# Kernel tuning notes

Hardware: AMD Instinct MI355X
Metric: run time of the kernel (lower is better)

Reference implementation:

```python
import jax, jax.numpy as jnp
import numpy as np
import math

D_MODEL = 1024
NUM_HEADS = 16
D_K = D_MODEL // NUM_HEADS
MAX_LEN = 2048
B, S = 2, 1024


def setup_inputs() -> dict:
    key = jax.random.key(0)
    ks = jax.random.split(key, 10)
    lin_scale = 1.0 / math.sqrt(D_MODEL)
    # torch Linear: weight (out, in), y = x @ W.T + b
    Wq = jax.random.uniform(ks[0], (D_MODEL, D_MODEL), jnp.float32, -lin_scale, lin_scale)
    Wk = jax.random.uniform(ks[1], (D_MODEL, D_MODEL), jnp.float32, -lin_scale, lin_scale)
    Wv = jax.random.uniform(ks[2], (D_MODEL, D_MODEL), jnp.float32, -lin_scale, lin_scale)
    Wo = jax.random.uniform(ks[3], (D_MODEL, D_MODEL), jnp.float32, -lin_scale, lin_scale)
    bq = jnp.zeros((D_MODEL,), jnp.float32)
    bk = jnp.zeros((D_MODEL,), jnp.float32)
    bv = jnp.zeros((D_MODEL,), jnp.float32)
    bo = jnp.zeros((D_MODEL,), jnp.float32)
    # xavier_uniform for Er (max_len, d_k)
    er_bound = math.sqrt(6.0 / (MAX_LEN + D_K))
    Er = jax.random.uniform(ks[4], (MAX_LEN, D_K), jnp.float32, -er_bound, er_bound)
    x = jax.random.normal(ks[5], (B, S, D_MODEL), jnp.float32)
    return {"x": x, "Wq": Wq, "bq": bq, "Wk": Wk, "bk": bk,
            "Wv": Wv, "bv": bv, "Wo": Wo, "bo": bo, "Er": Er}


def reference(x, Wq, bq, Wk, bk, Wv, bv, Wo, bo, Er):
    Bsz, Slen, Dm = x.shape
    H, dk = NUM_HEADS, D_K

    def proj(W, b):
        y = jnp.einsum('bsd,ed->bse', x, W) + b
        return y.reshape(Bsz, Slen, H, dk).transpose(0, 2, 1, 3)  # (B,H,S,dk)

    Q = proj(Wq, bq)
    K = proj(Wk, bk)
    V = proj(Wv, bv)

    # content-content scores
    AC = jnp.einsum('bhid,bhjd->bhij', Q, K)  # (B,H,S,S)

    # relative position embeddings for distances S-1 .. -(S-1)
    rel_pos = jnp.arange(Slen - 1, -Slen, -1)  # (2S-1,)
    idx = rel_pos + (Slen - 1)                 # map to 0..2S-2 (requires 2S-1 <= max_len)
    Er_emb = Er[idx]                           # (2S-1, dk)
    BD_full = jnp.einsum('bhid,md->bhim', Q, Er_emb)  # (B,H,S,2S-1)

    # relative shift: final[i,j] = BD_full[i, S-1 - i + j] (column for distance i-j)
    i_idx = jnp.arange(Slen)[:, None]                  # (S,1)
    m_idx = (Slen - 1) - i_idx + jnp.arange(Slen)[None, :]  # (S,S)
    BD = BD_full[:, :, i_idx, m_idx]                   # (B,H,S,S)

    scores = (AC + BD) / math.sqrt(dk)
    attn = jax.nn.softmax(scores, axis=-1)  # dropout is identity at eval
    out = jnp.einsum('bhij,bhjd->bhid', attn, V)       # (B,H,S,dk)
    out = out.transpose(0, 2, 1, 3).reshape(Bsz, Slen, Dm)
    return jnp.einsum('bsd,ed->bse', out, Wo) + bo
```

## Files before the change

kernel.cpp:

```cpp
#include <hip/hip_runtime.h>
#include <hip/hip_bf16.h>
#include <math.h>

#define D_MODEL 1024
#define NUM_HEADS 16
#define D_K 64
#define SEQ 1024
#define BATCH 2

typedef __hip_bfloat16 bf16;
typedef __bf16 bf16x8 __attribute__((ext_vector_type(8)));
typedef __bf16 bf16x4 __attribute__((ext_vector_type(4)));
typedef float floatx4 __attribute__((ext_vector_type(4)));

__device__ __forceinline__ floatx4 mfma16(bf16x8 a, bf16x8 b, floatx4 c) {
    return __builtin_amdgcn_mfma_f32_16x16x32_bf16(a, b, c, 0, 0, 0);
}

__global__ void detect_dtype_kernel(const void* __restrict__ x, int* __restrict__ flag) {
    __shared__ int cnt[256];
    const float* xf = (const float*)x;
    const int tid = threadIdx.x;
    int sane = 0;
    for (int i = tid; i < 4096; i += 256) {
        float v = xf[i];
        float a = fabsf(v);
        if (v == 0.0f || (a > 1e-8f && a < 1e8f)) sane++;
    }
    cnt[tid] = sane;
    __syncthreads();
    for (int s = 128; s > 0; s >>= 1) {
        if (tid < s) cnt[tid] += cnt[tid + s];
        __syncthreads();
    }
    if (tid == 0) flag[0] = (cnt[0] > 3686) ? 1 : 0;
}

struct ConvSrcs { const void* p[10]; };

__global__ __launch_bounds__(256) void convert_all_kernel(ConvSrcs srcs,
                                                          bf16* __restrict__ dstbase,
                                                          const int* __restrict__ flag) {
    const long long e = ((long long)blockIdx.x * 256 + threadIdx.x) * 8;
    int seg; long long base;
    if      (e < 2097152LL) { seg = 0; base = 0; }
    else if (e < 3145728LL) { seg = 1; base = 2097152LL; }
    else if (e < 4194304LL) { seg = 2; base = 3145728LL; }
    else if (e < 5242880LL) { seg = 3; base = 4194304LL; }
    else if (e < 6291456LL) { seg = 4; base = 5242880LL; }
    else if (e < 6292480LL) { seg = 5; base = 6291456LL; }
    else if (e < 6293504LL) { seg = 6; base = 6292480LL; }
    else if (e < 6294528LL) { seg = 7; base = 6293504LL; }
    else if (e < 6295552LL) { seg = 8; base = 6294528LL; }
    else                    { seg = 9; base = 6295552LL; }
    const long long local = e - base;
    __bf16 tmp[8];
    if (*flag) {
        const float* s = (const float*)srcs.p[seg] + local;
#pragma unroll
        for (int t = 0; t < 8; ++t) tmp[t] = (__bf16)s[t];
        *(bf16x8*)(void*)(dstbase + e) = *(const bf16x8*)tmp;
    } else {
        *(bf16x8*)(void*)(dstbase + e) =
            *(const bf16x8*)(const void*)((const bf16*)srcs.p[seg] + local);
    }
}

__global__ __launch_bounds__(256) void gemm_qkv_kernel(const bf16* __restrict__ x,
        const bf16* __restrict__ Wq, const bf16* __restrict__ Wk, const bf16* __restrict__ Wv,
        const bf16* __restrict__ bq, const bf16* __restrict__ bk, const bf16* __restrict__ bv,
        bf16* __restrict__ Qb, bf16* __restrict__ Kb, bf16* __restrict__ Vt) {
    const int wsel = blockIdx.x >> 4;
    const int n0 = (blockIdx.x & 15) * 64;
    const int m0 = blockIdx.y * 128;
    const bf16* W    = (wsel == 0) ? Wq : ((wsel == 1) ? Wk : Wv);
    const bf16* bias = (wsel == 0) ? bq : ((wsel == 1) ? bk : bv);

    __shared__ __bf16 As[128][72];
    __shared__ __bf16 Bs[64][72];
    const int tid = threadIdx.x;
    const int wave = tid >> 6, lane = tid & 63, quad = lane >> 4, l16 = lane & 15;
    const int wr = (wave >> 1) * 64, wc = (wave & 1) * 32;
    const int arow = tid >> 1, acg = (tid & 1) * 32;
    const int brow = tid >> 2, bcg = (tid & 3) * 16;

    floatx4 acc[4][2];
#pragma unroll
    for (int r = 0; r < 4; ++r)
#pragma unroll
        for (int c = 0; c < 2; ++c) acc[r][c] = (floatx4)0.f;

    for (int k0 = 0; k0 < 1024; k0 += 64) {
        const bf16* ag = x + (size_t)(m0 + arow) * 1024 + k0 + acg;
        const bf16* bg = W + (size_t)(n0 + brow) * 1024 + k0 + bcg;
        bf16x8 av[4], bv2[2];
#pragma unroll
        for (int c = 0; c < 4; ++c) av[c] = *(const bf16x8*)(const void*)(ag + c * 8);
#pragma unroll
        for (int c = 0; c < 2; ++c) bv2[c] = *(const bf16x8*)(const void*)(bg + c * 8);
        __syncthreads();
#pragma unroll
        for (int c = 0; c < 4; ++c) *(bf16x8*)&As[arow][acg + c * 8] = av[c];
#pragma unroll
        for (int c = 0; c < 2; ++c) *(bf16x8*)&Bs[brow][bcg + c * 8] = bv2[c];
        __syncthreads();
#pragma unroll
        for (int kk = 0; kk < 2; ++kk) {
            bf16x8 af[4], bfr[2];
#pragma unroll
            for (int r = 0; r < 4; ++r)
                af[r] = *(const bf16x8*)&As[wr + r * 16 + l16][kk * 32 + quad * 8];
#pragma unroll
            for (int c = 0; c < 2; ++c)
                bfr[c] = *(const bf16x8*)&Bs[wc + c * 16 + l16][kk * 32 + quad * 8];
#pragma unroll
            for (int r = 0; r < 4; ++r)
#pragma unroll
                for (int c = 0; c < 2; ++c)
                    acc[r][c] = mfma16(af[r], bfr[c], acc[r][c]);
        }
    }

    if (wsel < 2) {
        bf16* Cb = (wsel == 0) ? Qb : Kb;
#pragma unroll
        for (int c = 0; c < 2; ++c) {
            const int col = n0 + wc + c * 16 + l16;
            const float bvl = (float)bias[col];
#pragma unroll
            for (int r = 0; r < 4; ++r)
#pragma unroll
                for (int v = 0; v < 4; ++v) {
                    const int row = m0 + wr + r * 16 + quad * 4 + v;
                    Cb[(size_t)row * 1024 + col] = (bf16)(acc[r][c][v] + bvl);
                }
        }
    } else {
        __bf16* Ls = &As[0][0];
        __syncthreads();
#pragma unroll
        for (int c = 0; c < 2; ++c) {
            const int col = wc + c * 16 + l16;
            const float bvl = (float)bias[n0 + col];
#pragma unroll
            for (int r = 0; r < 4; ++r)
#pragma unroll
                for (int v = 0; v < 4; ++v) {
                    const int row = wr + r * 16 + quad * 4 + v;
                    Ls[col * 132 + row] = (__bf16)(acc[r][c][v] + bvl);
                }
        }
        __syncthreads();
        const int b = m0 >> 10, s0 = m0 & 1023, h = n0 >> 6;
        const int d = tid >> 2, sg = (tid & 3) * 32;
        bf16* g = Vt + ((size_t)((b * NUM_HEADS + h) * 64 + d)) * SEQ + s0 + sg;
#pragma unroll
        for (int c = 0; c < 32; c += 8)
            *(bf16x8*)(void*)(g + c) = *(const bf16x8*)&Ls[d * 132 + sg + c];
    }
}

__global__ __launch_bounds__(256, 3) void attn_mfma_kernel(const bf16* __restrict__ Q,
                                                           const bf16* __restrict__ Kc,
                                                           const bf16* __restrict__ Vt,
                                                           const bf16* __restrict__ Er,
                                                           bf16* __restrict__ Opart,
                                                           float* __restrict__ Ml) {
    const int i0 = blockIdx.x * 128;
    const int h = blockIdx.y;
    const int b = blockIdx.z >> 2, jsel = blockIdx.z & 3;
    const int tid = threadIdx.x;
    const int wave = tid >> 6, lane = tid & 63, quad = lane >> 4, l16 = lane & 15;

    __shared__ __bf16 Ks[64][72];
    __shared__ __bf16 Vs[80][72];
    __shared__ __bf16 scr_all[4][3264];
    __bf16* scr = &scr_all[wave][0];
    __bf16* Qs = &scr_all[0][0];

    for (int e = tid; e < 16 * 72; e += 256) {
        const int r = e / 72, c = e - r * 72;
        Vs[64 + r][c] = (r == 0) ? (__bf16)1.0f : (__bf16)0.0f;
    }
    {
        const int r = tid >> 1, cg = (tid & 1) * 32;
        const bf16* g = Q + ((size_t)(b * SEQ + i0 + r)) * D_MODEL + h * 64 + cg;
#pragma unroll
        for (int c = 0; c < 32; c += 8)
            *(bf16x8*)(void*)(Qs + r * 72 + cg + c) = *(const bf16x8*)(const void*)(g + c);
    }
    __syncthreads();
    bf16x8 aq[2][2];
#pragma unroll
    for (int half = 0; half < 2; ++half)
#pragma unroll
        for (int kk = 0; kk < 2; ++kk)
            aq[half][kk] = *(const bf16x8*)(const void*)(
                Qs + (wave * 32 + half * 16 + l16) * 72 + kk * 32 + quad * 8);

    floatx4 oacc[5][2];
#pragma unroll
    for (int ct = 0; ct < 5; ++ct)
#pragma unroll
        for (int half = 0; half < 2; ++half) oacc[ct][half] = (floatx4)0.f;

    const int eb = 960 + i0;
    const bf16* Kg = Kc + (size_t)b * SEQ * D_MODEL + h * 64;
    const bf16* Vtg = Vt + (size_t)((b * NUM_HEADS + h) * 64) * SEQ;
    const int jbeg = jsel * 256;

    const int r4 = tid >> 2, c4 = (tid & 3) * 16;
    bf16x8 kp0, kp1, vp0, vp1;
    {
        const bf16* kg = Kg + (size_t)(jbeg + r4) * D_MODEL + c4;
        const bf16* vg = Vtg + (size_t)r4 * SEQ + jbeg + c4;
        kp0 = *(const bf16x8*)(const void*)kg;
        kp1 = *(const bf16x8*)(const void*)(kg + 8);
        vp0 = *(const bf16x8*)(const void*)vg;
        vp1 = *(const bf16x8*)(const void*)(vg + 8);
    }

    for (int t = 0; t < 4; ++t) {
        const int j0 = jbeg + t * 64;
        __syncthreads();
        *(bf16x8*)&Ks[r4][c4]     = kp0;
        *(bf16x8*)&Ks[r4][c4 + 8] = kp1;
        *(bf16x8*)&Vs[r4][c4]     = vp0;
        *(bf16x8*)&Vs[r4][c4 + 8] = vp1;
        __syncthreads();
        if (t < 3) {
            const int jn = j0 + 64;
            const bf16* kg = Kg + (size_t)(jn + r4) * D_MODEL + c4;
            const bf16* vg = Vtg + (size_t)r4 * SEQ + jn + c4;
            kp0 = *(const bf16x8*)(const void*)kg;
            kp1 = *(const bf16x8*)(const void*)(kg + 8);
            vp0 = *(const bf16x8*)(const void*)vg;
            vp1 = *(const bf16x8*)(const void*)(vg + 8);
        }

#pragma unroll
        for (int ct = 0; ct < 6; ++ct) {
            const int erow = eb - j0 + wave * 32 + ct * 16 + l16;
            const bf16* ep = Er + (size_t)erow * 64 + quad * 8;
            bf16x8 be0 = *(const bf16x8*)(const void*)ep;
            bf16x8 be1 = *(const bf16x8*)(const void*)(ep + 32);
#pragma unroll
            for (int half = 0; half < 2; ++half) {
                floatx4 tv = (floatx4)0.f;
                tv = mfma16(aq[half][0], be0, tv);
                tv = mfma16(aq[half][1], be1, tv);
                bf16x4 tb;
#pragma unroll
                for (int v = 0; v < 4; ++v) tb[v] = (__bf16)tv[v];
                *(bf16x4*)(void*)(scr + (ct * 16 + l16) * 34 + half * 16 + quad * 4) = tb;
            }
        }
        floatx4 sfrag[4][2];
#pragma unroll
        for (int ct = 0; ct < 4; ++ct) {
            bf16x8 bk0 = *(const bf16x8*)&Ks[ct * 16 + l16][quad * 8];
            bf16x8 bk1 = *(const bf16x8*)&Ks[ct * 16 + l16][32 + quad * 8];
#pragma unroll
            for (int half = 0; half < 2; ++half) {
                floatx4 s = (floatx4)0.f;
                s = mfma16(aq[half][0], bk0, s);
                s = mfma16(aq[half][1], bk1, s);
                sfrag[ct][half] = s;
            }
        }
#pragma unroll
        for (int ct = 0; ct < 4; ++ct)
#pragma unroll
            for (int half = 0; half < 2; ++half)
#pragma unroll
                for (int v = 0; v < 4; ++v) {
                    const int rl = half * 16 + quad * 4 + v;
                    const int cl = 63 + rl - (ct * 16 + l16);
                    sfrag[ct][half][v] =
                        (sfrag[ct][half][v] + (float)scr[cl * 34 + rl]) * 0.125f;
                }
#pragma unroll
        for (int ct = 0; ct < 4; ++ct)
#pragma unroll
            for (int half = 0; half < 2; ++half)
#pragma unroll
                for (int v = 0; v < 4; ++v) {
                    const int rl = half * 16 + quad * 4 + v;
                    scr[rl * 72 + ct * 16 + l16] = (__bf16)__expf(sfrag[ct][half][v]);
                }
        bf16x8 ap[2][2];
#pragma unroll
        for (int half = 0; half < 2; ++half)
#pragma unroll
            for (int kk = 0; kk < 2; ++kk)
                ap[half][kk] = *(const bf16x8*)(const void*)(
                    scr + (half * 16 + l16) * 72 + kk * 32 + quad * 8);
#pragma unroll
        for (int ct = 0; ct < 5; ++ct) {
            bf16x8 bv0 = *(const bf16x8*)&Vs[ct * 16 + l16][quad * 8];
            bf16x8 bv1 = *(const bf16x8*)&Vs[ct * 16 + l16][32 + quad * 8];
#pragma unroll
            for (int half = 0; half < 2; ++half) {
                oacc[ct][half] = mfma16(ap[half][0], bv0, oacc[ct][half]);
                oacc[ct][half] = mfma16(ap[half][1], bv1, oacc[ct][half]);
            }
        }
    }

    bf16* Op = Opart + (size_t)jsel * 2097152;
#pragma unroll
    for (int ct = 0; ct < 4; ++ct)
#pragma unroll
        for (int half = 0; half < 2; ++half)
#pragma unroll
            for (int v = 0; v < 4; ++v) {
                const int row = i0 + wave * 32 + half * 16 + quad * 4 + v;
                const int col = h * 64 + ct * 16 + l16;
                Op[((size_t)(b * SEQ + row)) * D_MODEL + col] = (bf16)oacc[ct][half][v];
            }
    if (l16 == 0) {
        const int base = ((jsel * 2 + b) * 16 + h) * 1024;
#pragma unroll
        for (int half = 0; half < 2; ++half)
#pragma unroll
            for (int v = 0; v < 4; ++v) {
                const int ig = i0 + wave * 32 + half * 16 + quad * 4 + v;
                Ml[base + ig] = oacc[4][half][v];
            }
    }
}

__global__ __launch_bounds__(256) void gemm_out_kernel(const bf16* __restrict__ Opart,
        const float* __restrict__ Ml, const bf16* __restrict__ W,
        const bf16* __restrict__ bias, void* __restrict__ C,
        const int* __restrict__ flag) {
    const int n0 = blockIdx.x * 64;
    const int m0 = blockIdx.y * 64;
    __shared__ __bf16 As[64][72];
    __shared__ __bf16 Bs[64][72];
    __shared__ float Linv[64][16];
    const int tid = threadIdx.x;
    const int wave = tid >> 6, lane = tid & 63, quad = lane >> 4, l16 = lane & 15;
    const int wr = (wave >> 1) * 32, wc = (wave & 1) * 32;
    const int srow = tid >> 2, scg = (tid & 3) * 16;

    for (int e = tid; e < 1024; e += 256) {
        const int rl = e >> 4, hh = e & 15;
        const int row = m0 + rl, bb = row >> 10, ii = row & 1023;
        float l = 0.f;
#pragma unroll
        for (int s = 0; s < 4; ++s) l += Ml[(((s * 2 + bb) * 16 + hh) << 10) + ii];
        Linv[rl][hh] = 1.0f / l;
    }
    __syncthreads();

    floatx4 acc[2][2];
#pragma unroll
    for (int r = 0; r < 2; ++r)
#pragma unroll
        for (int c = 0; c < 2; ++c) acc[r][c] = (floatx4)0.f;

    for (int k0 = 0; k0 < 1024; k0 += 64) {
        const size_t aoff = (size_t)(m0 + srow) * 1024 + k0 + scg;
        const bf16* bg = W + (size_t)(n0 + srow) * 1024 + k0 + scg;
        bf16x8 o[4][2];
#pragma unroll
        for (int s = 0; s < 4; ++s) {
            o[s][0] = *(const bf16x8*)(const void*)(Opart + (size_t)s * 2097152 + aoff);
            o[s][1] = *(const bf16x8*)(const void*)(Opart + (size_t)s * 2097152 + aoff + 8);
        }
        bf16x8 bv0 = *(const bf16x8*)(const void*)bg;
        bf16x8 bv1 = *(const bf16x8*)(const void*)(bg + 8);
        const float linv = Linv[srow][(k0 + scg) >> 6];
        bf16x8 a0, a1;
#pragma unroll
        for (int t = 0; t < 8; ++t) {
            a0[t] = (__bf16)(((float)o[0][0][t] + (float)o[1][0][t] +
                              (float)o[2][0][t] + (float)o[3][0][t]) * linv);
            a1[t] = (__bf16)(((float)o[0][1][t] + (float)o[1][1][t] +
                              (float)o[2][1][t] + (float)o[3][1][t]) * linv);
        }
        __syncthreads();
        *(bf16x8*)&As[srow][scg]     = a0;
        *(bf16x8*)&As[srow][scg + 8] = a1;
        *(bf16x8*)&Bs[srow][scg]     = bv0;
        *(bf16x8*)&Bs[srow][scg + 8] = bv1;
        __syncthreads();
#pragma unroll
        for (int kk = 0; kk < 2; ++kk) {
            bf16x8 af[2], bfr[2];
#pragma unroll
            for (int r = 0; r < 2; ++r)
                af[r] = *(const bf16x8*)&As[wr + r * 16 + l16][kk * 32 + quad * 8];
#pragma unroll
            for (int c = 0; c < 2; ++c)
                bfr[c] = *(const bf16x8*)&Bs[wc + c * 16 + l16][kk * 32 + quad * 8];
#pragma unroll
            for (int r = 0; r < 2; ++r)
#pragma unroll
                for (int c = 0; c < 2; ++c)
                    acc[r][c] = mfma16(af[r], bfr[c], acc[r][c]);
        }
    }
#pragma unroll
    for (int c = 0; c < 2; ++c) {
        const int col = n0 + wc + c * 16 + l16;
        const float bvl = (float)bias[col];
#pragma unroll
        for (int r = 0; r < 2; ++r)
#pragma unroll
            for (int v = 0; v < 4; ++v) {
                const int row = m0 + wr + r * 16 + quad * 4 + v;
                const float val = acc[r][c][v] + bvl;
                const size_t idx = (size_t)row * 1024 + col;
                if (*flag) ((float*)C)[idx] = val;
                else       ((bf16*)C)[idx] = (bf16)val;
            }
    }
}

extern "C" void kernel_launch(void* const* d_in, const int* in_sizes, int n_in,
                              void* d_out, int out_size, void* d_ws, size_t ws_size,
                              hipStream_t stream) {
    const size_t E_X = 2097152;
    const size_t E_CANON = 6426624;

    char* ws = (char*)d_ws;
    int* flag = (int*)ws;
    bf16* canon = (bf16*)(ws + 16);
    bf16* xc  = canon;
    bf16* Wqc = canon + 2097152;
    bf16* Wkc = canon + 3145728;
    bf16* Wvc = canon + 4194304;
    bf16* Woc = canon + 5242880;
    bf16* bqc = canon + 6291456;
    bf16* bkc = canon + 6292480;
    bf16* bvc = canon + 6293504;
    bf16* boc = canon + 6294528;
    bf16* Erc = canon + 6295552;
    bf16* p = canon + E_CANON;
    bf16* Qb    = p;  p += E_X;
    bf16* Kb    = p;  p += E_X;
    bf16* Vt    = p;  p += E_X;
    bf16* Opart = p;  p += 4 * E_X;
    float* Ml   = (float*)p;

    detect_dtype_kernel<<<1, 256, 0, stream>>>(d_in[0], flag);

    ConvSrcs cs;
    cs.p[0] = d_in[0]; cs.p[1] = d_in[1]; cs.p[2] = d_in[3]; cs.p[3] = d_in[5];
    cs.p[4] = d_in[7]; cs.p[5] = d_in[2]; cs.p[6] = d_in[4]; cs.p[7] = d_in[6];
    cs.p[8] = d_in[8]; cs.p[9] = d_in[9];
    convert_all_kernel<<<3138, 256, 0, stream>>>(cs, canon, flag);

    gemm_qkv_kernel<<<dim3(48, 16), 256, 0, stream>>>(xc, Wqc, Wkc, Wvc,
                                                      bqc, bkc, bvc, Qb, Kb, Vt);

    attn_mfma_kernel<<<dim3(8, 16, 8), 256, 0, stream>>>(Qb, Kb, Vt, Erc, Opart, Ml);

    gemm_out_kernel<<<dim3(16, 32), 256, 0, stream>>>(Opart, Ml, Woc, boc, d_out, flag);
}
```

Measured before the change: 215.7 us.

## Split attention keys into three uneven chunks and add separate combine kernel

The attention kernel now splits the 1024 keys into 3 chunks (384/320/320) instead of 4 equal ones, giving 768 blocks rather than 1024 and one fewer partial output buffer. The split-K merge and normalisation move out of the output GEMM into a standalone combine kernel that writes the merged result into the Q buffer. The output GEMM then reads only one A tile per step instead of four partials with inline scaling. The cost is an extra kernel launch and an extra round trip to memory for the combined activations, plus uneven per-block work in attention.

```diff
diff --git a/kernel.cpp b/kernel.cpp
--- a/kernel.cpp
+++ b/kernel.cpp
@@ -168,9 +168,13 @@
                                                            float* __restrict__ Ml) {
     const int i0 = blockIdx.x * 128;
     const int h = blockIdx.y;
-    const int b = blockIdx.z >> 2, jsel = blockIdx.z & 3;
+    const int zz = blockIdx.z;
+    const int b = zz / 3, jsel = zz - b * 3;
     const int tid = threadIdx.x;
     const int wave = tid >> 6, lane = tid & 63, quad = lane >> 4, l16 = lane & 15;
+
+    const int jbeg = (jsel == 0) ? 0 : ((jsel == 1) ? 384 : 704);
+    const int nt   = (jsel == 0) ? 6 : 5;
 
     __shared__ __bf16 Ks[64][72];
     __shared__ __bf16 Vs[80][72];
@@ -207,7 +211,6 @@
     const int eb = 960 + i0;
     const bf16* Kg = Kc + (size_t)b * SEQ * D_MODEL + h * 64;
     const bf16* Vtg = Vt + (size_t)((b * NUM_HEADS + h) * 64) * SEQ;
-    const int jbeg = jsel * 256;
 
     const int r4 = tid >> 2, c4 = (tid & 3) * 16;
     bf16x8 kp0, kp1, vp0, vp1;
@@ -220,7 +223,7 @@
         vp1 = *(const bf16x8*)(const void*)(vg + 8);
     }
 
-    for (int t = 0; t < 4; ++t) {
+    for (int t = 0; t < nt; ++t) {
         const int j0 = jbeg + t * 64;
         __syncthreads();
         *(bf16x8*)&Ks[r4][c4]     = kp0;
@@ -228,7 +231,7 @@
         *(bf16x8*)&Vs[r4][c4]     = vp0;
         *(bf16x8*)&Vs[r4][c4 + 8] = vp1;
         __syncthreads();
-        if (t < 3) {
+        if (t < nt - 1) {
             const int jn = j0 + 64;
             const bf16* kg = Kg + (size_t)(jn + r4) * D_MODEL + c4;
             const bf16* vg = Vtg + (size_t)r4 * SEQ + jn + c4;
@@ -330,30 +333,38 @@
     }
 }
 
-__global__ __launch_bounds__(256) void gemm_out_kernel(const bf16* __restrict__ Opart,
-        const float* __restrict__ Ml, const bf16* __restrict__ W,
-        const bf16* __restrict__ bias, void* __restrict__ C,
-        const int* __restrict__ flag) {
+__global__ __launch_bounds__(256) void combine_kernel(const bf16* __restrict__ Opart,
+                                                      const float* __restrict__ Ml,
+                                                      bf16* __restrict__ Ob) {
+    const int e = (blockIdx.x * 256 + threadIdx.x) * 4;
+    const int row = e >> 10, col = e & 1023;
+    const int b = row >> 10, i = row & 1023, h = col >> 6;
+    float l = 0.f;
+#pragma unroll
+    for (int s = 0; s < 3; ++s) l += Ml[(((s * 2 + b) * 16 + h) << 10) + i];
+    const float inv = 1.0f / l;
+    bf16x4 o1 = *(const bf16x4*)(const void*)(Opart + e);
+    bf16x4 o2 = *(const bf16x4*)(const void*)(Opart + 2097152 + e);
+    bf16x4 o3 = *(const bf16x4*)(const void*)(Opart + 4194304 + e);
+    bf16x4 o;
+#pragma unroll
+    for (int v = 0; v < 4; ++v)
+        o[v] = (__bf16)(((float)o1[v] + (float)o2[v] + (float)o3[v]) * inv);
+    *(bf16x4*)(void*)(Ob + e) = o;
+}
+
+__global__ __launch_bounds__(256) void gemm_out_kernel(const bf16* __restrict__ A,
+        const bf16* __restrict__ W, const bf16* __restrict__ bias,
+        void* __restrict__ C, const int* __restrict__ flag) {
     const int n0 = blockIdx.x * 64;
     const int m0 = blockIdx.y * 64;
     __shared__ __bf16 As[64][72];
     __shared__ __bf16 Bs[64][72];
-    __shared__ float Linv[64][16];
     const int tid = threadIdx.x;
     const int wave = tid >> 6, lane = tid & 63, quad = lane >> 4, l16 = lane & 15;
     const int wr = (wave >> 1) * 32, wc = (wave & 1) * 32;
     const int srow = tid >> 2, scg = (tid & 3) * 16;
 
-    for (int e = tid; e < 1024; e += 256) {
-        const int rl = e >> 4, hh = e & 15;
-        const int row = m0 + rl, bb = row >> 10, ii = row & 1023;
-        float l = 0.f;
-#pragma unroll
-        for (int s = 0; s < 4; ++s) l += Ml[(((s * 2 + bb) * 16 + hh) << 10) + ii];
-        Linv[rl][hh] = 1.0f / l;
-    }
-    __syncthreads();
-
     floatx4 acc[2][2];
 #pragma unroll
     for (int r = 0; r < 2; ++r)
@@ -361,28 +372,15 @@
         for (int c = 0; c < 2; ++c) acc[r][c] = (floatx4)0.f;
 
     for (int k0 = 0; k0 < 1024; k0 += 64) {
-        const size_t aoff = (size_t)(m0 + srow) * 1024 + k0 + scg;
+        const bf16* ag = A + (size_t)(m0 + srow) * 1024 + k0 + scg;
         const bf16* bg = W + (size_t)(n0 + srow) * 1024 + k0 + scg;
-        bf16x8 o[4][2];
-#pragma unroll
-        for (int s = 0; s < 4; ++s) {
-            o[s][0] = *(const bf16x8*)(const void*)(Opart + (size_t)s * 2097152 + aoff);
-            o[s][1] = *(const bf16x8*)(const void*)(Opart + (size_t)s * 2097152 + aoff + 8);
-        }
+        bf16x8 av0 = *(const bf16x8*)(const void*)ag;
+        bf16x8 av1 = *(const bf16x8*)(const void*)(ag + 8);
         bf16x8 bv0 = *(const bf16x8*)(const void*)bg;
         bf16x8 bv1 = *(const bf16x8*)(const void*)(bg + 8);
-        const float linv = Linv[srow][(k0 + scg) >> 6];
-        bf16x8 a0, a1;
-#pragma unroll
-        for (int t = 0; t < 8; ++t) {
-            a0[t] = (__bf16)(((float)o[0][0][t] + (float)o[1][0][t] +
-                              (float)o[2][0][t] + (float)o[3][0][t]) * linv);
-            a1[t] = (__bf16)(((float)o[0][1][t] + (float)o[1][1][t] +
-                              (float)o[2][1][t] + (float)o[3][1][t]) * linv);
-        }
-        __syncthreads();
-        *(bf16x8*)&As[srow][scg]     = a0;
-        *(bf16x8*)&As[srow][scg + 8] = a1;
+        __syncthreads();
+        *(bf16x8*)&As[srow][scg]     = av0;
+        *(bf16x8*)&As[srow][scg + 8] = av1;
         *(bf16x8*)&Bs[srow][scg]     = bv0;
         *(bf16x8*)&Bs[srow][scg + 8] = bv1;
         __syncthreads();
@@ -442,7 +440,7 @@
     bf16* Qb    = p;  p += E_X;
     bf16* Kb    = p;  p += E_X;
     bf16* Vt    = p;  p += E_X;
-    bf16* Opart = p;  p += 4 * E_X;
+    bf16* Opart = p;  p += 3 * E_X;
     float* Ml   = (float*)p;
 
     detect_dtype_kernel<<<1, 256, 0, stream>>>(d_in[0], flag);
@@ -456,7 +454,9 @@
     gemm_qkv_kernel<<<dim3(48, 16), 256, 0, stream>>>(xc, Wqc, Wkc, Wvc,
                                                       bqc, bkc, bvc, Qb, Kb, Vt);
 
-    attn_mfma_kernel<<<dim3(8, 16, 8), 256, 0, stream>>>(Qb, Kb, Vt, Erc, Opart, Ml);
-
-    gemm_out_kernel<<<dim3(16, 32), 256, 0, stream>>>(Opart, Ml, Woc, boc, d_out, flag);
-}
+    attn_mfma_kernel<<<dim3(8, 16, 6), 256, 0, stream>>>(Qb, Kb, Vt, Erc, Opart, Ml);
+
+    combine_kernel<<<2048, 256, 0, stream>>>(Opart, Ml, Qb);
+
+    gemm_out_kernel<<<dim3(16, 32), 256, 0, stream>>>(Qb, Woc, boc, d_out, flag);
+}
```

Measured after the change: 187.8 us. -12.9%, faster.
